# Kernel optimization log

Measured on AMD Instinct MI355X. Metric: run time of the kernel, lower is better.

Reference implementation:

```python
import jax, jax.numpy as jnp
import numpy as np

B, N, D, A, R, E = 4, 50000, 128, 128, 200, 600000  # batch, entities, hidden dim, attn dim, relations, edges


def setup_inputs() -> dict:
    key = jax.random.key(0)
    ks = jax.random.split(key, 18)
    sD = 1.0 / np.sqrt(D)
    sA = 1.0 / np.sqrt(A)
    id_bat = jax.random.randint(ks[0], (E,), 0, B)
    id_sub = id_bat * N + jax.random.randint(ks[1], (E,), 0, N)
    id_rel = jax.random.randint(ks[2], (E,), 0, R)
    id_obj = id_bat * N + jax.random.randint(ks[3], (E,), 0, N)
    edges = jnp.stack([id_bat, id_sub, id_rel, id_obj], axis=1)
    return {
        "query": jax.random.normal(ks[4], (B, D), jnp.float32),
        "q_sub": jax.random.randint(ks[5], (B,), 0, N),
        "q_rel": jax.random.randint(ks[6], (B,), 0, R),
        "hidden": jax.random.normal(ks[7], (B, N, D), jnp.float32),
        "edges": edges,
        "nodes": jax.random.randint(ks[8], (B, 2), 0, N),
        "Ws_attn_w": jax.random.normal(ks[9], (A, D), jnp.float32) * sD,
        "Wr_attn_w": jax.random.normal(ks[10], (A, D), jnp.float32) * sD,
        "Wqr_attn_w": jax.random.normal(ks[11], (A, D), jnp.float32) * sD,
        "Wqr_attn_b": jax.random.normal(ks[12], (A,), jnp.float32) * sD,
        "W_attn_w": jax.random.normal(ks[13], (1, A), jnp.float32) * sA,
        "rela_embed": jax.random.normal(ks[14], (R, D), jnp.float32) * sD,
        "mlp1_w": jax.random.normal(ks[15], (D, D), jnp.float32) * sD,
        "mlp1_b": jnp.zeros((D,), jnp.float32),
        "mlp2_w": jax.random.normal(ks[16], (D, D), jnp.float32) * sD,
        "mlp2_b": jnp.zeros((D,), jnp.float32),
    }


def reference(query, q_sub, q_rel, hidden, edges, nodes,
              Ws_attn_w, Wr_attn_w, Wqr_attn_w, Wqr_attn_b, W_attn_w,
              rela_embed, mlp1_w, mlp1_b, mlp2_w, mlp2_b):
    b, n, d = hidden.shape
    id_bat, id_sub, id_rel, id_obj = edges[:, 0], edges[:, 1], edges[:, 2], edges[:, 3]
    all_ent = hidden.reshape(b * n, d)                       # [B*N, D]
    mh = all_ent[id_sub]                                     # [E, D] gather heads
    mr = rela_embed[id_rel]                                  # [E, D] gather relations
    mq = query[id_bat]                                       # [E, D] gather queries
    mess = mh * mr                                           # distmult message
    # attention MLP: sigmoid(W_attn @ relu(Ws h + Wr r + Wqr q + b))
    h_attn = jax.nn.relu(mh @ Ws_attn_w.T + mr @ Wr_attn_w.T + mq @ Wqr_attn_w.T + Wqr_attn_b)
    alpha = jax.nn.sigmoid(h_attn @ W_attn_w.T)              # [E, 1]
    message = mess * alpha
    # scatter-sum aggregate over destination nodes
    agg = jax.ops.segment_sum(message, id_obj, num_segments=b * n)   # [B*N, D]
    # mask of nodes that received at least one message (== torch.unique(id_obj))
    deg = jax.ops.segment_sum(jnp.ones((id_obj.shape[0],), jnp.float32), id_obj, num_segments=b * n)
    recv = deg > 0                                           # [B*N]
    # per-row MLP: Linear -> Linear -> ReLU (mlp_num=2, no activation between)
    h = jax.nn.relu((agg @ mlp1_w.T + mlp1_b) @ mlp2_w.T + mlp2_b)
    new_hidden = jnp.where(recv[:, None], h, 0.0).reshape(b, n, d)
    return new_hidden
```

## Files before the change

### kernel.cpp

```cpp
#include <hip/hip_runtime.h>

typedef unsigned int u32;
typedef unsigned short u16;
typedef unsigned long long u64;
typedef __attribute__((ext_vector_type(8))) short bf16x8;
typedef __attribute__((ext_vector_type(4))) float f32x4;

#define Bb 4
#define Nn 50000
#define Dd 128
#define Rr 200
#define BN (Bb*Nn)
#define MAXDEG 16
#define LDW 136
#define SLAB 4352

__device__ __forceinline__ float bfs(u16 u) { return __uint_as_float(((u32)u) << 16); }
__device__ __forceinline__ float bflo(u32 u) { return __uint_as_float(u << 16); }
__device__ __forceinline__ float bfhi(u32 u) { return __uint_as_float(u & 0xffff0000u); }
__device__ __forceinline__ u16 f2bf(float f) {
    u32 x = __float_as_uint(f);
    return (u16)((x + 0x7fffu + ((x >> 16) & 1u)) >> 16);
}
template<bool BF>
__device__ __forceinline__ float ld1(const void* p, int i) {
    if (BF) return bfs(((const u16*)p)[i]);
    else    return ((const float*)p)[i];
}

__global__ void k_probe(const u32* __restrict__ q, int* __restrict__ flag) {
    int t = threadIdx.x;
    u32 w = q[t];
    int e = (int)((w >> 7) & 0xffu);
    bool plaus = (e >= 100 && e <= 150);
    unsigned long long m = __ballot(plaus);
    if (t == 0) flag[0] = (__popcll(m) >= 56) ? 1 : 0;
}

__global__ __launch_bounds__(256) void k_wprep(
    const void* Ws, const void* w1, const void* w2,
    const void* b1, const void* b2, const void* wattn, const void* rela,
    u16* WsH, u16* WsL, u16* w1H, u16* w1L, u16* w2H, u16* w2L,
    float* b1f, float* b2f, float* wattnf, float* relaf, const int* flag) {
    bool bf = (*flag != 0);
    int i = blockIdx.x * 256 + threadIdx.x;
    if (i < 16384) {
        float x = bf ? bfs(((const u16*)Ws)[i]) : ((const float*)Ws)[i];
        u16 h = f2bf(x); WsH[i] = h; WsL[i] = f2bf(x - bfs(h));
    } else if (i < 32768) {
        int j = i - 16384;
        float x = bf ? bfs(((const u16*)w1)[j]) : ((const float*)w1)[j];
        u16 h = f2bf(x); w1H[j] = h; w1L[j] = f2bf(x - bfs(h));
    } else if (i < 49152) {
        int j = i - 32768;
        float x = bf ? bfs(((const u16*)w2)[j]) : ((const float*)w2)[j];
        u16 h = f2bf(x); w2H[j] = h; w2L[j] = f2bf(x - bfs(h));
    } else if (i < 49152 + 128) {
        int j = i - 49152;
        b1f[j] = bf ? bfs(((const u16*)b1)[j]) : ((const float*)b1)[j];
    } else if (i < 49152 + 256) {
        int j = i - 49152 - 128;
        b2f[j] = bf ? bfs(((const u16*)b2)[j]) : ((const float*)b2)[j];
    } else if (i < 49152 + 384) {
        int j = i - 49152 - 256;
        wattnf[j] = bf ? bfs(((const u16*)wattn)[j]) : ((const float*)wattn)[j];
    } else if (i < 49152 + 384 + 25600) {
        int j = i - 49152 - 384;
        relaf[j] = bf ? bfs(((const u16*)rela)[j]) : ((const float*)rela)[j];
    }
}

template<bool BF>
__device__ __forceinline__ float dotrow1(const void* W, int row, const float* s) {
    float acc = 0.f;
    if (BF) {
        const uint4* wv = (const uint4*)((const u16*)W + row * Dd);
#pragma unroll
        for (int k = 0; k < 16; k++) {
            uint4 u = wv[k];
            acc += bflo(u.x)*s[k*8+0] + bfhi(u.x)*s[k*8+1]
                 + bflo(u.y)*s[k*8+2] + bfhi(u.y)*s[k*8+3]
                 + bflo(u.z)*s[k*8+4] + bfhi(u.z)*s[k*8+5]
                 + bflo(u.w)*s[k*8+6] + bfhi(u.w)*s[k*8+7];
        }
    } else {
        const float4* wv = (const float4*)((const float*)W + row * Dd);
#pragma unroll
        for (int k = 0; k < 32; k++) {
            float4 u = wv[k];
            acc += u.x*s[4*k] + u.y*s[4*k+1] + u.z*s[4*k+2] + u.w*s[4*k+3];
        }
    }
    return acc;
}
template<bool BF>
__device__ void k_wrq_body(const void* Wr, const void* Wqr, const void* bias,
                           const void* rela, const void* query, float* wrq, float* s) {
    int br = blockIdx.x;
    int b = br / Rr, r = br % Rr;
    int a = threadIdx.x;
    s[a]      = ld1<BF>(rela,  r * Dd + a);
    s[Dd + a] = ld1<BF>(query, b * Dd + a);
    __syncthreads();
    wrq[br * Dd + a] = ld1<BF>(bias, a) + dotrow1<BF>(Wr, a, s) + dotrow1<BF>(Wqr, a, s + Dd);
}
__global__ __launch_bounds__(128) void k_wrq(const void* Wr, const void* Wqr, const void* bias,
                                             const void* rela, const void* query, float* wrq,
                                             const int* flag) {
    __shared__ float s[2 * Dd];
    if (*flag) k_wrq_body<true>(Wr, Wqr, bias, rela, query, wrq, s);
    else       k_wrq_body<false>(Wr, Wqr, bias, rela, query, wrq, s);
}

template<bool BF>
__device__ void hs_body(const void* hidden, const u16* WsH, const u16* WsL, u16* hs,
                        u16* __restrict__ Smh) {
    int t = threadIdx.x, lane = t & 63;
    int m16 = lane & 15, quad = lane >> 4;
    int w = t >> 6;
    int base = blockIdx.x * 64 + w * 16;
    u16* Sml = Smh + 16 * LDW;

    if (BF) {
        const u16* src = (const u16*)hidden + (size_t)base * Dd;
#pragma unroll
        for (int j = 0; j < 4; j++) {
            int flat = j * 64 + lane;
            int row = flat >> 4, c8 = (flat & 15) * 8;
            uint4 v = ((const uint4*)src)[flat];
            *(uint4*)(Smh + row * LDW + c8) = v;
        }
    } else {
        const float* src = (const float*)hidden + (size_t)base * Dd;
#pragma unroll
        for (int j = 0; j < 8; j++) {
            int flat = j * 64 + lane;
            int row = flat >> 5, c4 = (flat & 31) * 4;
            float4 v = ((const float4*)src)[flat];
            u16 h0 = f2bf(v.x), h1 = f2bf(v.y), h2 = f2bf(v.z), h3 = f2bf(v.w);
            ushort4 hv; hv.x = h0; hv.y = h1; hv.z = h2; hv.w = h3;
            ushort4 lv; lv.x = f2bf(v.x - bfs(h0)); lv.y = f2bf(v.y - bfs(h1));
                        lv.z = f2bf(v.z - bfs(h2)); lv.w = f2bf(v.w - bfs(h3));
            *(ushort4*)(Smh + row * LDW + c4) = hv;
            *(ushort4*)(Sml + row * LDW + c4) = lv;
        }
    }
    const u16* ph = Smh + m16 * LDW + quad * 8;
    const u16* pl = Sml + m16 * LDW + quad * 8;
    bf16x8 ah[4], al[4];
#pragma unroll
    for (int ks = 0; ks < 4; ks++) {
        ah[ks] = *(const bf16x8*)(ph + ks * 32);
        if (!BF) al[ks] = *(const bf16x8*)(pl + ks * 32);
    }
#pragma unroll
    for (int nt = 0; nt < 8; nt++) {
        int n = nt * 16 + m16;
        f32x4 acc = {0.f, 0.f, 0.f, 0.f};
#pragma unroll
        for (int ks = 0; ks < 4; ks++) {
            bf16x8 bh = *(const bf16x8*)(WsH + n * Dd + ks * 32 + quad * 8);
            acc = __builtin_amdgcn_mfma_f32_16x16x32_bf16(ah[ks], bh, acc, 0, 0, 0);
            if (!BF) {
                bf16x8 bl = *(const bf16x8*)(WsL + n * Dd + ks * 32 + quad * 8);
                acc = __builtin_amdgcn_mfma_f32_16x16x32_bf16(al[ks], bh, acc, 0, 0, 0);
                acc = __builtin_amdgcn_mfma_f32_16x16x32_bf16(ah[ks], bl, acc, 0, 0, 0);
            }
        }
#pragma unroll
        for (int r = 0; r < 4; r++)
            hs[(size_t)(base + quad * 4 + r) * Dd + n] = f2bf(acc[r]);
    }
}
__global__ __launch_bounds__(256, 4) void k_hs(const void* hidden, const u16* WsH,
                                               const u16* WsL, u16* hs, const int* flag) {
    __shared__ __align__(16) u16 SL[4][SLAB];
    u16* slab = SL[threadIdx.x >> 6];
    if (*flag) hs_body<true>(hidden, WsH, WsL, hs, slab);
    else       hs_body<false>(hidden, WsH, WsL, hs, slab);
}

__global__ __launch_bounds__(256) void k_alpha(const int* __restrict__ edges,
                                               const u16* __restrict__ hs,
                                               const float* __restrict__ wrq,
                                               const float* __restrict__ wattnf,
                                               u64* __restrict__ slotsAL,
                                               int* __restrict__ deg, int nE) {
    int tid = blockIdx.x * 256 + threadIdx.x;
    int g = tid >> 4, l = tid & 15;
    if (g >= nE) return;
    int4 ed = ((const int4*)edges)[g];
    const u16*   hp = hs  + (size_t)ed.y * Dd + l * 8;
    const float* wp = wrq + (size_t)(ed.x * Rr + ed.z) * Dd + l * 8;
    uint4  hv = *(const uint4*)hp;
    float4 w0 = *(const float4*)wp;
    float4 w1 = *(const float4*)(wp + 4);
    float4 a0 = *(const float4*)(wattnf + l * 8);
    float4 a1 = *(const float4*)(wattnf + l * 8 + 4);
    float p = fmaxf(bflo(hv.x) + w0.x, 0.f) * a0.x + fmaxf(bfhi(hv.x) + w0.y, 0.f) * a0.y
            + fmaxf(bflo(hv.y) + w0.z, 0.f) * a0.z + fmaxf(bfhi(hv.y) + w0.w, 0.f) * a0.w
            + fmaxf(bflo(hv.z) + w1.x, 0.f) * a1.x + fmaxf(bfhi(hv.z) + w1.y, 0.f) * a1.y
            + fmaxf(bflo(hv.w) + w1.z, 0.f) * a1.z + fmaxf(bfhi(hv.w) + w1.w, 0.f) * a1.w;
#pragma unroll
    for (int m = 8; m >= 1; m >>= 1) p += __shfl_xor(p, m, 16);
    if (l == 0) {
        float alpha = 1.f / (1.f + __expf(-p));
        int pos = atomicAdd(&deg[ed.w], 1);
        if (pos < MAXDEG) {
            u32 rec = (u32)ed.y | ((u32)ed.z << 18);
            slotsAL[(size_t)ed.w * MAXDEG + pos] =
                (u64)rec | ((u64)__float_as_uint(alpha) << 32);
        }
    }
}

template<bool BF>
__device__ __forceinline__ void gfma(u32 rec, float al, int lane,
                                     const void* __restrict__ hidden,
                                     const float* __restrict__ relaf,
                                     float& a0, float& a1) {
    int sub = rec & 0x3FFFF, rel = (rec >> 18) & 0xFF;
    float mh0, mh1;
    if (BF) { u32 mh = ((const u32*)hidden)[(size_t)sub * 64 + lane]; mh0 = bflo(mh); mh1 = bfhi(mh); }
    else    { float2 mh = ((const float2*)hidden)[(size_t)sub * 64 + lane]; mh0 = mh.x; mh1 = mh.y; }
    float2 mr = ((const float2*)relaf)[rel * 64 + lane];
    a0 += mh0 * mr.x * al;
    a1 += mh1 * mr.y * al;
}

template<bool BF>
__device__ void fused_body(const u64* __restrict__ slotsAL, const int* __restrict__ deg,
                           const void* __restrict__ hidden, const float* __restrict__ relaf,
                           const u16* w1H, const u16* w1L, const u16* w2H, const u16* w2L,
                           const float* b1f, const float* b2f, void* out,
                           u16* __restrict__ Smh, char* __restrict__ SB) {
    int t = threadIdx.x, lane = t & 63;
    int m16 = lane & 15, quad = lane >> 4;
    int w = t >> 6;
    int base = blockIdx.x * 64 + w * 16;
    u16* Sml = Smh + 16 * LDW;

    {
        const uint4* sp = (const uint4*)((const char*)(slotsAL + (size_t)base * MAXDEG)
                                         + (size_t)(lane >> 2) * (MAXDEG * 8) + (lane & 3) * 16);
        *(uint4*)(SB + lane * 16) = *sp;
    }

    for (int i = 0; i < 16; i += 2) {
        int nA = base + i, nB = nA + 1;
        int dA = deg[nA]; if (dA > MAXDEG) dA = MAXDEG;
        int dB = deg[nB]; if (dB > MAXDEG) dB = MAXDEG;
        const char* pA = SB + i * 64;
        const char* pB = pA + 64;
        float aA0 = 0.f, aA1 = 0.f, aB0 = 0.f, aB1 = 0.f;

#pragma unroll
        for (int e = 0; e < 4; e++) {
            uint2 qA = *(const uint2*)(pA + e * 8);
            uint2 qB = *(const uint2*)(pB + e * 8);
            u32  rA = (e < dA) ? qA.x : 0u;
            float lA = (e < dA) ? __uint_as_float(qA.y) : 0.f;
            u32  rB = (e < dB) ? qB.x : 0u;
            float lB = (e < dB) ? __uint_as_float(qB.y) : 0.f;
            gfma<BF>(rA, lA, lane, hidden, relaf, aA0, aA1);
            gfma<BF>(rB, lB, lane, hidden, relaf, aB0, aB1);
        }
        if (dA > 4 || dB > 4) {
#pragma unroll
            for (int e = 4; e < 8; e++) {
                uint2 qA = *(const uint2*)(pA + e * 8);
                uint2 qB = *(const uint2*)(pB + e * 8);
                u32  rA = (e < dA) ? qA.x : 0u;
                float lA = (e < dA) ? __uint_as_float(qA.y) : 0.f;
                u32  rB = (e < dB) ? qB.x : 0u;
                float lB = (e < dB) ? __uint_as_float(qB.y) : 0.f;
                gfma<BF>(rA, lA, lane, hidden, relaf, aA0, aA1);
                gfma<BF>(rB, lB, lane, hidden, relaf, aB0, aB1);
            }
        }
        for (int e = 8; e < dA; e++) {
            u64 q = slotsAL[(size_t)nA * MAXDEG + e];
            gfma<BF>((u32)q, __uint_as_float((u32)(q >> 32)), lane, hidden, relaf, aA0, aA1);
        }
        for (int e = 8; e < dB; e++) {
            u64 q = slotsAL[(size_t)nB * MAXDEG + e];
            gfma<BF>((u32)q, __uint_as_float((u32)(q >> 32)), lane, hidden, relaf, aB0, aB1);
        }

        u16 hA0 = f2bf(aA0), lA0 = f2bf(aA0 - bfs(hA0));
        u16 hA1 = f2bf(aA1), lA1 = f2bf(aA1 - bfs(hA1));
        *(u32*)(Smh + i * LDW + 2 * lane) = (u32)hA0 | ((u32)hA1 << 16);
        *(u32*)(Sml + i * LDW + 2 * lane) = (u32)lA0 | ((u32)lA1 << 16);
        u16 hB0 = f2bf(aB0), lB0 = f2bf(aB0 - bfs(hB0));
        u16 hB1 = f2bf(aB1), lB1 = f2bf(aB1 - bfs(hB1));
        *(u32*)(Smh + (i + 1) * LDW + 2 * lane) = (u32)hB0 | ((u32)hB1 << 16);
        *(u32*)(Sml + (i + 1) * LDW + 2 * lane) = (u32)lB0 | ((u32)lB1 << 16);
    }

    const u16* ph = Smh + m16 * LDW + quad * 8;
    const u16* pl = Sml + m16 * LDW + quad * 8;
    bf16x8 ah[4], al[4];
#pragma unroll
    for (int ks = 0; ks < 4; ks++) {
        ah[ks] = *(const bf16x8*)(ph + ks * 32);
        al[ks] = *(const bf16x8*)(pl + ks * 32);
    }
#pragma unroll
    for (int nt = 0; nt < 8; nt++) {
        int n = nt * 16 + m16;
        f32x4 acc = {0.f, 0.f, 0.f, 0.f};
#pragma unroll
        for (int ks = 0; ks < 4; ks++) {
            bf16x8 bh = *(const bf16x8*)(w1H + n * Dd + ks * 32 + quad * 8);
            acc = __builtin_amdgcn_mfma_f32_16x16x32_bf16(ah[ks], bh, acc, 0, 0, 0);
            acc = __builtin_amdgcn_mfma_f32_16x16x32_bf16(al[ks], bh, acc, 0, 0, 0);
            if (!BF) {
                bf16x8 bl = *(const bf16x8*)(w1L + n * Dd + ks * 32 + quad * 8);
                acc = __builtin_amdgcn_mfma_f32_16x16x32_bf16(ah[ks], bl, acc, 0, 0, 0);
            }
        }
        float bv = b1f[n];
#pragma unroll
        for (int r = 0; r < 4; r++) {
            float v = acc[r] + bv;
            int row = quad * 4 + r;
            u16 h = f2bf(v);
            Smh[row * LDW + n] = h;
            Sml[row * LDW + n] = f2bf(v - bfs(h));
        }
    }

    bf16x8 mh[4], ml[4];
#pragma unroll
    for (int ks = 0; ks < 4; ks++) {
        mh[ks] = *(const bf16x8*)(ph + ks * 32);
        ml[ks] = *(const bf16x8*)(pl + ks * 32);
    }
    int dg[4];
#pragma unroll
    for (int r = 0; r < 4; r++) dg[r] = deg[base + quad * 4 + r];
#pragma unroll
    for (int nt = 0; nt < 8; nt++) {
        int n = nt * 16 + m16;
        f32x4 acc = {0.f, 0.f, 0.f, 0.f};
#pragma unroll
        for (int ks = 0; ks < 4; ks++) {
            bf16x8 bh = *(const bf16x8*)(w2H + n * Dd + ks * 32 + quad * 8);
            acc = __builtin_amdgcn_mfma_f32_16x16x32_bf16(mh[ks], bh, acc, 0, 0, 0);
            acc = __builtin_amdgcn_mfma_f32_16x16x32_bf16(ml[ks], bh, acc, 0, 0, 0);
            if (!BF) {
                bf16x8 bl = *(const bf16x8*)(w2L + n * Dd + ks * 32 + quad * 8);
                acc = __builtin_amdgcn_mfma_f32_16x16x32_bf16(mh[ks], bl, acc, 0, 0, 0);
            }
        }
        float bv = b2f[n];
#pragma unroll
        for (int r = 0; r < 4; r++) {
            float v = fmaxf(acc[r] + bv, 0.f);
            if (dg[r] == 0) v = 0.f;
            size_t o = (size_t)(base + quad * 4 + r) * Dd + n;
            if (BF) ((u16*)out)[o] = f2bf(v);
            else    ((float*)out)[o] = v;
        }
    }
}
__global__ __launch_bounds__(256, 4) void k_fused(const u64* slotsAL, const int* deg,
                                                  const void* hidden, const float* relaf,
                                                  const u16* w1H, const u16* w1L,
                                                  const u16* w2H, const u16* w2L,
                                                  const float* b1f, const float* b2f,
                                                  void* out, const int* flag) {
    __shared__ __align__(16) u16 SL[4][SLAB];
    __shared__ __align__(16) char SBL[4][1024];
    int w = threadIdx.x >> 6;
    if (*flag) fused_body<true>(slotsAL, deg, hidden, relaf,
                                w1H, w1L, w2H, w2L, b1f, b2f, out, SL[w], SBL[w]);
    else       fused_body<false>(slotsAL, deg, hidden, relaf,
                                 w1H, w1L, w2H, w2L, b1f, b2f, out, SL[w], SBL[w]);
}

extern "C" void kernel_launch(void* const* d_in, const int* in_sizes, int n_in,
                              void* d_out, int out_size, void* d_ws, size_t ws_size,
                              hipStream_t stream) {
    const void* query  = d_in[0];
    const void* hidden = d_in[3];
    const int*  edges  = (const int*)d_in[4];
    const void* Ws     = d_in[6];
    const void* Wr     = d_in[7];
    const void* Wqr    = d_in[8];
    const void* Wqrb   = d_in[9];
    const void* Wattn  = d_in[10];
    const void* rela   = d_in[11];
    const void* w1     = d_in[12];
    const void* b1     = d_in[13];
    const void* w2     = d_in[14];
    const void* b2     = d_in[15];

    char* ws = (char*)d_ws;
    u16*   hs     = (u16*)ws;
    float* wrq    = (float*)(ws +  51200000);
    u64*   slotsAL= (u64*) (ws +  51609600);
    int*   deg    = (int*) (ws +  77209600);
    u16*   WsH    = (u16*) (ws +  78009600);
    u16*   WsL    = (u16*) (ws +  78042368);
    u16*   w1H    = (u16*) (ws +  78075136);
    u16*   w1L    = (u16*) (ws +  78107904);
    u16*   w2H    = (u16*) (ws +  78140672);
    u16*   w2L    = (u16*) (ws +  78173440);
    float* b1f    = (float*)(ws +  78206208);
    float* b2f    = (float*)(ws +  78206720);
    float* wattnf = (float*)(ws +  78207232);
    float* relaf  = (float*)(ws +  78207744);
    int*   flag   = (int*) (ws +  78310144);

    int nE = in_sizes[4] / 4;

    k_probe<<<1, 64, 0, stream>>>((const u32*)query, flag);
    hipMemsetAsync(deg, 0, (size_t)BN * 4, stream);
    k_wprep<<<294, 256, 0, stream>>>(Ws, w1, w2, b1, b2, Wattn, rela,
                                     WsH, WsL, w1H, w1L, w2H, w2L,
                                     b1f, b2f, wattnf, relaf, flag);
    k_wrq<<<Bb * Rr, 128, 0, stream>>>(Wr, Wqr, Wqrb, rela, query, wrq, flag);
    k_hs<<<BN / 64, 256, 0, stream>>>(hidden, WsH, WsL, hs, flag);
    {
        long long thr = (long long)nE * 16;
        int blocks = (int)((thr + 255) / 256);
        k_alpha<<<blocks, 256, 0, stream>>>(edges, hs, wrq, wattnf, slotsAL, deg, nE);
    }
    k_fused<<<BN / 64, 256, 0, stream>>>(slotsAL, deg, hidden, relaf,
                                         w1H, w1L, w2H, w2L, b1f, b2f, d_out, flag);
}
```

Measured before the change: 665.1 us.

## Drop low-part split of activations in fused MLP and inline dtype probe

The fused MLP kernel stops splitting the aggregated activations and the intermediate MLP output into bf16 high/low pairs. Only the high part is kept, which removes one MFMA per k-step in both GEMMs and halves the shared-memory slab, so occupancy bounds rise to 6 blocks. The separate probe kernel is removed and each kernel recomputes the dtype check inline from the query tensor, saving one launch. The cost is lower precision on the activation side of the fp32 path, which risks larger errors.

Result: no change. 671.6 us (+1.0%).

```diff
diff --git a/kernel.cpp b/kernel.cpp
--- a/kernel.cpp
+++ b/kernel.cpp
@@ -13,7 +13,7 @@
 #define BN (Bb*Nn)
 #define MAXDEG 16
 #define LDW 136
-#define SLAB 4352
+#define SLAB 2176
 
 __device__ __forceinline__ float bfs(u16 u) { return __uint_as_float(((u32)u) << 16); }
 __device__ __forceinline__ float bflo(u32 u) { return __uint_as_float(u << 16); }
@@ -28,21 +28,22 @@
     else    return ((const float*)p)[i];
 }
 
-__global__ void k_probe(const u32* __restrict__ q, int* __restrict__ flag) {
-    int t = threadIdx.x;
-    u32 w = q[t];
+__device__ __forceinline__ bool probe_bf(const void* query) {
+    int lane = threadIdx.x & 63;
+    u32 w = ((const u32*)query)[lane];
     int e = (int)((w >> 7) & 0xffu);
     bool plaus = (e >= 100 && e <= 150);
     unsigned long long m = __ballot(plaus);
-    if (t == 0) flag[0] = (__popcll(m) >= 56) ? 1 : 0;
+    return __popcll(m) >= 56;
 }
 
 __global__ __launch_bounds__(256) void k_wprep(
+    const void* query,
     const void* Ws, const void* w1, const void* w2,
     const void* b1, const void* b2, const void* wattn, const void* rela,
     u16* WsH, u16* WsL, u16* w1H, u16* w1L, u16* w2H, u16* w2L,
-    float* b1f, float* b2f, float* wattnf, float* relaf, const int* flag) {
-    bool bf = (*flag != 0);
+    float* b1f, float* b2f, float* wattnf, float* relaf) {
+    bool bf = probe_bf(query);
     int i = blockIdx.x * 256 + threadIdx.x;
     if (i < 16384) {
         float x = bf ? bfs(((const u16*)Ws)[i]) : ((const float*)Ws)[i];
@@ -105,11 +106,10 @@
     wrq[br * Dd + a] = ld1<BF>(bias, a) + dotrow1<BF>(Wr, a, s) + dotrow1<BF>(Wqr, a, s + Dd);
 }
 __global__ __launch_bounds__(128) void k_wrq(const void* Wr, const void* Wqr, const void* bias,
-                                             const void* rela, const void* query, float* wrq,
-                                             const int* flag) {
+                                             const void* rela, const void* query, float* wrq) {
     __shared__ float s[2 * Dd];
-    if (*flag) k_wrq_body<true>(Wr, Wqr, bias, rela, query, wrq, s);
-    else       k_wrq_body<false>(Wr, Wqr, bias, rela, query, wrq, s);
+    if (probe_bf(query)) k_wrq_body<true>(Wr, Wqr, bias, rela, query, wrq, s);
+    else                 k_wrq_body<false>(Wr, Wqr, bias, rela, query, wrq, s);
 }
 
 template<bool BF>
@@ -173,11 +173,11 @@
     }
 }
 __global__ __launch_bounds__(256, 4) void k_hs(const void* hidden, const u16* WsH,
-                                               const u16* WsL, u16* hs, const int* flag) {
-    __shared__ __align__(16) u16 SL[4][SLAB];
+                                               const u16* WsL, u16* hs, const void* query) {
+    __shared__ __align__(16) u16 SL[4][2 * SLAB];
     u16* slab = SL[threadIdx.x >> 6];
-    if (*flag) hs_body<true>(hidden, WsH, WsL, hs, slab);
-    else       hs_body<false>(hidden, WsH, WsL, hs, slab);
+    if (probe_bf(query)) hs_body<true>(hidden, WsH, WsL, hs, slab);
+    else                 hs_body<false>(hidden, WsH, WsL, hs, slab);
 }
 
 __global__ __launch_bounds__(256) void k_alpha(const int* __restrict__ edges,
@@ -238,7 +238,6 @@
     int m16 = lane & 15, quad = lane >> 4;
     int w = t >> 6;
     int base = blockIdx.x * 64 + w * 16;
-    u16* Sml = Smh + 16 * LDW;
 
     {
         const uint4* sp = (const uint4*)((const char*)(slotsAL + (size_t)base * MAXDEG)
@@ -287,24 +286,17 @@
             gfma<BF>((u32)q, __uint_as_float((u32)(q >> 32)), lane, hidden, relaf, aB0, aB1);
         }
 
-        u16 hA0 = f2bf(aA0), lA0 = f2bf(aA0 - bfs(hA0));
-        u16 hA1 = f2bf(aA1), lA1 = f2bf(aA1 - bfs(hA1));
+        u16 hA0 = f2bf(aA0), hA1 = f2bf(aA1);
         *(u32*)(Smh + i * LDW + 2 * lane) = (u32)hA0 | ((u32)hA1 << 16);
-        *(u32*)(Sml + i * LDW + 2 * lane) = (u32)lA0 | ((u32)lA1 << 16);
-        u16 hB0 = f2bf(aB0), lB0 = f2bf(aB0 - bfs(hB0));
-        u16 hB1 = f2bf(aB1), lB1 = f2bf(aB1 - bfs(hB1));
+        u16 hB0 = f2bf(aB0), hB1 = f2bf(aB1);
         *(u32*)(Smh + (i + 1) * LDW + 2 * lane) = (u32)hB0 | ((u32)hB1 << 16);
-        *(u32*)(Sml + (i + 1) * LDW + 2 * lane) = (u32)lB0 | ((u32)lB1 << 16);
     }
 
     const u16* ph = Smh + m16 * LDW + quad * 8;
-    const u16* pl = Sml + m16 * LDW + quad * 8;
-    bf16x8 ah[4], al[4];
-#pragma unroll
-    for (int ks = 0; ks < 4; ks++) {
+    bf16x8 ah[4];
+#pragma unroll
+    for (int ks = 0; ks < 4; ks++)
         ah[ks] = *(const bf16x8*)(ph + ks * 32);
-        al[ks] = *(const bf16x8*)(pl + ks * 32);
-    }
 #pragma unroll
     for (int nt = 0; nt < 8; nt++) {
         int n = nt * 16 + m16;
@@ -313,7 +305,6 @@
         for (int ks = 0; ks < 4; ks++) {
             bf16x8 bh = *(const bf16x8*)(w1H + n * Dd + ks * 32 + quad * 8);
             acc = __builtin_amdgcn_mfma_f32_16x16x32_bf16(ah[ks], bh, acc, 0, 0, 0);
-            acc = __builtin_amdgcn_mfma_f32_16x16x32_bf16(al[ks], bh, acc, 0, 0, 0);
             if (!BF) {
                 bf16x8 bl = *(const bf16x8*)(w1L + n * Dd + ks * 32 + quad * 8);
                 acc = __builtin_amdgcn_mfma_f32_16x16x32_bf16(ah[ks], bl, acc, 0, 0, 0);
@@ -324,18 +315,14 @@
         for (int r = 0; r < 4; r++) {
             float v = acc[r] + bv;
             int row = quad * 4 + r;
-            u16 h = f2bf(v);
-            Smh[row * LDW + n] = h;
-            Sml[row * LDW + n] = f2bf(v - bfs(h));
-        }
-    }
-
-    bf16x8 mh[4], ml[4];
-#pragma unroll
-    for (int ks = 0; ks < 4; ks++) {
+            Smh[row * LDW + n] = f2bf(v);
+        }
+    }
+
+    bf16x8 mh[4];
+#pragma unroll
+    for (int ks = 0; ks < 4; ks++)
         mh[ks] = *(const bf16x8*)(ph + ks * 32);
-        ml[ks] = *(const bf16x8*)(pl + ks * 32);
-    }
     int dg[4];
 #pragma unroll
     for (int r = 0; r < 4; r++) dg[r] = deg[base + quad * 4 + r];
@@ -347,7 +334,6 @@
         for (int ks = 0; ks < 4; ks++) {
             bf16x8 bh = *(const bf16x8*)(w2H + n * Dd + ks * 32 + quad * 8);
             acc = __builtin_amdgcn_mfma_f32_16x16x32_bf16(mh[ks], bh, acc, 0, 0, 0);
-            acc = __builtin_amdgcn_mfma_f32_16x16x32_bf16(ml[ks], bh, acc, 0, 0, 0);
             if (!BF) {
                 bf16x8 bl = *(const bf16x8*)(w2L + n * Dd + ks * 32 + quad * 8);
                 acc = __builtin_amdgcn_mfma_f32_16x16x32_bf16(mh[ks], bl, acc, 0, 0, 0);
@@ -364,18 +350,18 @@
         }
     }
 }
-__global__ __launch_bounds__(256, 4) void k_fused(const u64* slotsAL, const int* deg,
+__global__ __launch_bounds__(256, 6) void k_fused(const u64* slotsAL, const int* deg,
                                                   const void* hidden, const float* relaf,
                                                   const u16* w1H, const u16* w1L,
                                                   const u16* w2H, const u16* w2L,
                                                   const float* b1f, const float* b2f,
-                                                  void* out, const int* flag) {
+                                                  void* out, const void* query) {
     __shared__ __align__(16) u16 SL[4][SLAB];
     __shared__ __align__(16) char SBL[4][1024];
     int w = threadIdx.x >> 6;
-    if (*flag) fused_body<true>(slotsAL, deg, hidden, relaf,
+    if (probe_bf(query)) fused_body<true>(slotsAL, deg, hidden, relaf,
                                 w1H, w1L, w2H, w2L, b1f, b2f, out, SL[w], SBL[w]);
-    else       fused_body<false>(slotsAL, deg, hidden, relaf,
+    else                 fused_body<false>(slotsAL, deg, hidden, relaf,
                                  w1H, w1L, w2H, w2L, b1f, b2f, out, SL[w], SBL[w]);
 }
 
@@ -411,22 +397,22 @@
     float* b2f    = (float*)(ws +  78206720);
     float* wattnf = (float*)(ws +  78207232);
     float* relaf  = (float*)(ws +  78207744);
-    int*   flag   = (int*) (ws +  78310144);
+    int*   flagUnused = (int*)(ws + 78310144);
+    (void)flagUnused;
 
     int nE = in_sizes[4] / 4;
 
-    k_probe<<<1, 64, 0, stream>>>((const u32*)query, flag);
     hipMemsetAsync(deg, 0, (size_t)BN * 4, stream);
-    k_wprep<<<294, 256, 0, stream>>>(Ws, w1, w2, b1, b2, Wattn, rela,
+    k_wprep<<<294, 256, 0, stream>>>(query, Ws, w1, w2, b1, b2, Wattn, rela,
                                      WsH, WsL, w1H, w1L, w2H, w2L,
-                                     b1f, b2f, wattnf, relaf, flag);
-    k_wrq<<<Bb * Rr, 128, 0, stream>>>(Wr, Wqr, Wqrb, rela, query, wrq, flag);
-    k_hs<<<BN / 64, 256, 0, stream>>>(hidden, WsH, WsL, hs, flag);
+                                     b1f, b2f, wattnf, relaf);
+    k_wrq<<<Bb * Rr, 128, 0, stream>>>(Wr, Wqr, Wqrb, rela, query, wrq);
+    k_hs<<<BN / 64, 256, 0, stream>>>(hidden, WsH, WsL, hs, query);
     {
         long long thr = (long long)nE * 16;
         int blocks = (int)((thr + 255) / 256);
         k_alpha<<<blocks, 256, 0, stream>>>(edges, hs, wrq, wattnf, slotsAL, deg, nE);
     }
     k_fused<<<BN / 64, 256, 0, stream>>>(slotsAL, deg, hidden, relaf,
-                                         w1H, w1L, w2H, w2L, b1f, b2f, d_out, flag);
-}
+                                         w1H, w1L, w2H, w2L, b1f, b2f, d_out, query);
+}
```
